# Optimization experiments

Hardware: AMD Instinct MI355X
Metric: run time of the kernel (lower is better)

The kernel has to match this reference:

```python
import jax, jax.numpy as jnp
import numpy as np

B, V, NQ, D, HEADS, FF, NL = 2, 8, 336, 256, 8, 1024, 6
H_IMG, W_IMG = 512, 512


def setup_inputs() -> dict:
    key = jax.random.key(0)
    ks = iter(jax.random.split(key, 48))
    def n(shape, s=0.02):
        return jax.random.normal(next(ks), shape, dtype=jnp.float32) * s
    inp = {}
    inp["tgt"] = jnp.zeros((B, NQ, D), jnp.float32)
    inp["query_pos"] = jax.random.normal(next(ks), (B, NQ, D), jnp.float32)
    inp["reference_points"] = jax.random.uniform(next(ks), (B, NQ, 3), dtype=jnp.float32)
    inp["feat0"] = jax.random.normal(next(ks), (B, V, D, 64, 64), jnp.float32)
    inp["feat1"] = jax.random.normal(next(ks), (B, V, D, 32, 32), jnp.float32)
    inp["feat2"] = jax.random.normal(next(ks), (B, V, D, 16, 16), jnp.float32)
    # cameras: near-identity rotations, translation pushed +2 in z so points project in front
    inp["camera_R"] = jnp.broadcast_to(jnp.eye(3, dtype=jnp.float32), (B, V, 3, 3)) + n((B, V, 3, 3), 0.1)
    T = n((B, V, 3), 0.1)
    inp["camera_T"] = T.at[..., 2].add(2.0)
    K = jnp.array([[500.0, 0.0, 256.0], [0.0, 500.0, 256.0], [0.0, 0.0, 1.0]], jnp.float32)
    inp["camera_K"] = jnp.broadcast_to(K, (B, V, 3, 3))
    # decoder params (stacked over NL layers)
    inp["Wqkv"] = n((NL, 3 * D, D)); inp["bqkv"] = jnp.zeros((NL, 3 * D), jnp.float32)
    inp["Wo"] = n((NL, D, D));       inp["bo"] = jnp.zeros((NL, D), jnp.float32)
    inp["ln1_g"] = jnp.ones((NL, D), jnp.float32); inp["ln1_b"] = jnp.zeros((NL, D), jnp.float32)
    inp["Wproj"] = n((NL, D, D));    inp["bproj"] = jnp.zeros((NL, D), jnp.float32)
    inp["pn_g"] = jnp.ones((NL, D), jnp.float32); inp["pn_b"] = jnp.zeros((NL, D), jnp.float32)
    inp["W1"] = n((NL, FF, D));      inp["b1"] = jnp.zeros((NL, FF), jnp.float32)
    inp["W2"] = n((NL, D, FF));      inp["b2"] = jnp.zeros((NL, D), jnp.float32)
    inp["ln2_g"] = jnp.ones((NL, D), jnp.float32); inp["ln2_b"] = jnp.zeros((NL, D), jnp.float32)
    inp["pose_W0"] = n((D, D)); inp["pose_b0"] = jnp.zeros((D,), jnp.float32)
    inp["pose_W1"] = n((D, D)); inp["pose_b1"] = jnp.zeros((D,), jnp.float32)
    inp["pose_W2"] = n((3, D)); inp["pose_b2"] = jnp.zeros((3,), jnp.float32)
    inp["cls_W"] = n((1, D));   inp["cls_b"] = jnp.zeros((1,), jnp.float32)
    return inp


def _layer_norm(x, g, b):
    m = x.mean(-1, keepdims=True)
    v = ((x - m) ** 2).mean(-1, keepdims=True)
    return (x - m) * jax.lax.rsqrt(v + 1e-5) * g + b


def _project(pts, R, T, K):
    # pts (B,NQ,3) -> cam coords per view: pts @ R^T + T
    p = jnp.einsum('bqc,bvdc->bvqd', pts, R) + T[:, :, None, :]  # (B,V,NQ,3)
    z = jnp.clip(p[..., 2], 0.1, None)
    fx = K[..., 0, 0][:, :, None]; fy = K[..., 1, 1][:, :, None]
    cx = K[..., 0, 2][:, :, None]; cy = K[..., 1, 2][:, :, None]
    u = p[..., 0] * fx / z + cx
    v = p[..., 1] * fy / z + cy
    un = 2.0 * u / (W_IMG - 1) - 1.0
    vn = 2.0 * v / (H_IMG - 1) - 1.0
    mask = (un > -1.0) & (un < 1.0) & (vn > -1.0) & (vn < 1.0) & (p[..., 2] > 0)
    return jnp.stack([un, vn], -1), mask  # (B,V,NQ,2), (B,V,NQ)


def _sample(feats, grid):
    # bilinear point sampling == F.grid_sample(align_corners=False, padding_mode='zeros')
    C, Hh, Ww = feats.shape[2], feats.shape[3], feats.shape[4]
    f = feats.reshape(B * V, C, Hh, Ww)
    g = grid.reshape(B * V, NQ, 2)
    x = (g[..., 0] + 1.0) * Ww * 0.5 - 0.5
    y = (g[..., 1] + 1.0) * Hh * 0.5 - 0.5
    x0f = jnp.floor(x); y0f = jnp.floor(y)
    ix0 = x0f.astype(jnp.int32); iy0 = y0f.astype(jnp.int32)
    ix1 = ix0 + 1; iy1 = iy0 + 1
    wx1 = (x - x0f)[:, None, :]; wx0 = 1.0 - wx1
    wy1 = (y - y0f)[:, None, :]; wy0 = 1.0 - wy1
    def gat(ix, iy):
        valid = ((ix >= 0) & (ix < Ww) & (iy >= 0) & (iy < Hh)).astype(f.dtype)[:, None, :]
        ixc = jnp.clip(ix, 0, Ww - 1); iyc = jnp.clip(iy, 0, Hh - 1)
        vals = jax.vmap(lambda ff, yy, xx: ff[:, yy, xx])(f, iyc, ixc)  # (BV,C,NQ)
        return vals * valid
    out = (gat(ix0, iy0) * wy0 * wx0 + gat(ix1, iy0) * wy0 * wx1 +
           gat(ix0, iy1) * wy1 * wx0 + gat(ix1, iy1) * wy1 * wx1)
    return out.reshape(B, V, C, NQ).transpose(0, 1, 3, 2)  # (B,V,NQ,C)


def _mha(xq, xv, Wqkv, bqkv, Wo, bo):
    hd = D // HEADS
    q = (xq @ Wqkv[:D].T + bqkv[:D]).reshape(B, NQ, HEADS, hd)
    k = (xq @ Wqkv[D:2 * D].T + bqkv[D:2 * D]).reshape(B, NQ, HEADS, hd)
    v = (xv @ Wqkv[2 * D:].T + bqkv[2 * D:]).reshape(B, NQ, HEADS, hd)
    att = jax.nn.softmax(jnp.einsum('bqhd,bkhd->bhqk', q, k) * (1.0 / np.sqrt(hd)), axis=-1)
    o = jnp.einsum('bhqk,bkhd->bqhd', att, v).reshape(B, NQ, D)
    return o @ Wo.T + bo


def reference(tgt, query_pos, reference_points, feat0, feat1, feat2, camera_R, camera_T, camera_K,
              Wqkv, bqkv, Wo, bo, ln1_g, ln1_b, Wproj, bproj, pn_g, pn_b,
              W1, b1, W2, b2, ln2_g, ln2_b,
              pose_W0, pose_b0, pose_W1, pose_b1, pose_W2, pose_b2, cls_W, cls_b):
    out = tgt
    ref = reference_points
    feats = (feat0, feat1, feat2)
    logits_all, poses_all = [], []
    for l in range(NL):
        # self-attention (dropout = eval identity)
        qk = out + query_pos
        out = _layer_norm(out + _mha(qk, out, Wqkv[l], bqkv[l], Wo[l], bo[l]), ln1_g[l], ln1_b[l])
        # projective attention: project 3D refs, grid-sample all levels, mask-fuse across views
        grid, mask = _project(ref, camera_R, camera_T, camera_K)
        ms = (_sample(feats[0], grid) + _sample(feats[1], grid) + _sample(feats[2], grid)) / 3.0
        vm = mask[..., None].astype(out.dtype)  # (B,V,NQ,1)
        fused = (ms * vm).sum(1) / jnp.clip(vm.sum(1), 1.0, None)  # (B,NQ,D)
        out = _layer_norm(out + fused @ Wproj[l].T + bproj[l], pn_g[l], pn_b[l])
        # FFN
        ffn = jax.nn.relu(out @ W1[l].T + b1[l]) @ W2[l].T + b2[l]
        out = _layer_norm(out + ffn, ln2_g[l], ln2_b[l])
        # iterative pose refinement + classification head
        h = jax.nn.relu(out @ pose_W0.T + pose_b0)
        h = jax.nn.relu(h @ pose_W1.T + pose_b1)
        ref = ref + h @ pose_W2.T + pose_b2
        logits_all.append(out @ cls_W.T + cls_b)
        poses_all.append(ref)
    # (NL,B,NQ,1) logits ++ (NL,B,NQ,3) poses -> (NL,B,NQ,4)
    return jnp.concatenate([jnp.stack(logits_all), jnp.stack(poses_all)], axis=-1)
```

## Files before the change

### kernel.cpp

```cpp
#include <hip/hip_runtime.h>
#include <math.h>

#define BB 2
#define VV 8
#define NQ 336
#define DD 256
#define HEADS 8
#define HD 32
#define FF 1024
#define NL 6
#define BQ (BB*NQ)
#define W_IMG 512
#define H_IMG 512
#define MROWS BQ

__device__ __forceinline__ void job_transpose3(float* tile, int b,
                                               const float* __restrict__ f0,
                                               const float* __restrict__ f1,
                                               const float* __restrict__ f2,
                                               float* __restrict__ o0,
                                               float* __restrict__ o1,
                                               float* __restrict__ o2) {
    const float* src; float* dst; int HW, ptiles;
    if (b < 4096)      { src = f0; dst = o0; HW = 4096; ptiles = 128; }
    else if (b < 5120) { b -= 4096; src = f1; dst = o1; HW = 1024; ptiles = 32; }
    else               { b -= 5120; src = f2; dst = o2; HW = 256;  ptiles = 8;  }
    int cg = b & 1;
    int pt = (b >> 1) % ptiles;
    int bv = (b >> 1) / ptiles;
    int d0 = cg * 128, p0 = pt * 32;
    int t = threadIdx.x;
    int chb = t >> 3, px4 = (t & 7) * 4;
    #pragma unroll
    for (int pass = 0; pass < 4; ++pass) {
        int ch = pass * 32 + chb;
        float4 v = *(const float4*)(src + ((size_t)(bv * DD + d0 + ch)) * HW + p0 + px4);
        tile[ch * 33 + px4 + 0] = v.x; tile[ch * 33 + px4 + 1] = v.y;
        tile[ch * 33 + px4 + 2] = v.z; tile[ch * 33 + px4 + 3] = v.w;
    }
    __syncthreads();
    int c4 = (t & 31) * 4, pxb = t >> 5;
    #pragma unroll
    for (int pass = 0; pass < 4; ++pass) {
        int px = pass * 8 + pxb;
        float4 o;
        o.x = tile[(c4 + 0) * 33 + px];
        o.y = tile[(c4 + 1) * 33 + px];
        o.z = tile[(c4 + 2) * 33 + px];
        o.w = tile[(c4 + 3) * 33 + px];
        *(float4*)(dst + ((size_t)bv * HW + p0 + px) * DD + d0 + c4) = o;
    }
}

__global__ __launch_bounds__(256) void init_k(const float* __restrict__ tgt,
                                              const float* __restrict__ qp,
                                              const float* __restrict__ refpts,
                                              float* __restrict__ x,
                                              float* __restrict__ xq,
                                              float* __restrict__ refb) {
    int i = blockIdx.x * 256 + threadIdx.x;
    float4 tv = ((const float4*)tgt)[i];
    float4 qv = ((const float4*)qp)[i];
    ((float4*)x)[i] = tv;
    ((float4*)xq)[i] = make_float4(tv.x + qv.x, tv.y + qv.y, tv.z + qv.z, tv.w + qv.w);
    if (i < BQ * 3) refb[i] = refpts[i];
}

__device__ __forceinline__ void job_qkv(float* sm, int bid,
                                        const float* __restrict__ Aq,
                                        const float* __restrict__ Ax,
                                        const float* __restrict__ W,
                                        const float* __restrict__ bias,
                                        float* __restrict__ Qp,
                                        float* __restrict__ Kp,
                                        float* __restrict__ Vp) {
    float* At = sm;
    float* Wt = sm + 1088;
    int t = threadIdx.x;
    int m0 = (bid % 21) * 32;
    int ncol = bid / 21;
    int n0 = ncol * 64;
    const float* A = (ncol < 8) ? Aq : Ax;
    int tx = t & 15, ty = t >> 4;
    int nc = n0 + tx * 4;
    float acc0[4], acc1[4];
    {
        float4 bv = *(const float4*)(bias + nc);
        acc0[0] = bv.x; acc0[1] = bv.y; acc0[2] = bv.z; acc0[3] = bv.w;
        acc1[0] = bv.x; acc1[1] = bv.y; acc1[2] = bv.z; acc1[3] = bv.w;
    }
    int am = t >> 3, ak4 = (t & 7) * 4;
    for (int kt = 0; kt < 8; ++kt) {
        int kk = kt * 32;
        __syncthreads();
        {
            float4 v = *(const float4*)(A + (size_t)(m0 + am) * DD + kk + ak4);
            At[(ak4 + 0) * 34 + am] = v.x; At[(ak4 + 1) * 34 + am] = v.y;
            At[(ak4 + 2) * 34 + am] = v.z; At[(ak4 + 3) * 34 + am] = v.w;
        }
        #pragma unroll
        for (int s = 0; s < 2; ++s) {
            int idx = t + s * 256;
            int wn = idx >> 3, wk4 = (idx & 7) * 4;
            float4 v = *(const float4*)(W + (size_t)(n0 + wn) * DD + kk + wk4);
            Wt[(wk4 + 0) * 68 + wn] = v.x; Wt[(wk4 + 1) * 68 + wn] = v.y;
            Wt[(wk4 + 2) * 68 + wn] = v.z; Wt[(wk4 + 3) * 68 + wn] = v.w;
        }
        __syncthreads();
        #pragma unroll
        for (int k = 0; k < 32; ++k) {
            float2 av = *(const float2*)&At[k * 34 + ty * 2];
            float4 wv = *(const float4*)&Wt[k * 68 + tx * 4];
            acc0[0] = fmaf(av.x, wv.x, acc0[0]); acc0[1] = fmaf(av.x, wv.y, acc0[1]);
            acc0[2] = fmaf(av.x, wv.z, acc0[2]); acc0[3] = fmaf(av.x, wv.w, acc0[3]);
            acc1[0] = fmaf(av.y, wv.x, acc1[0]); acc1[1] = fmaf(av.y, wv.y, acc1[1]);
            acc1[2] = fmaf(av.y, wv.z, acc1[2]); acc1[3] = fmaf(av.y, wv.w, acc1[3]);
        }
    }
    int mr = m0 + ty * 2;
    int kind = nc >> 8;
    float* base = kind == 0 ? Qp : (kind == 1 ? Kp : Vp);
    int h = (nc >> 5) & 7, d4 = nc & 31;
    #pragma unroll
    for (int i = 0; i < 2; ++i) {
        int m = mr + i;
        int b = m / NQ, q = m - b * NQ;
        float* p = base + ((size_t)((b << 3) + h) * NQ + q) * HD + d4;
        float* src = i == 0 ? acc0 : acc1;
        *(float4*)p = make_float4(src[0], src[1], src[2], src[3]);
    }
}

__device__ __forceinline__ void job_pose(float* sm, int job,
                                         const float* __restrict__ x,
                                         const float* __restrict__ W0, const float* __restrict__ b0,
                                         const float* __restrict__ W1p, const float* __restrict__ b1p,
                                         const float* __restrict__ W2p, const float* __restrict__ b2p,
                                         const float* __restrict__ cW, const float* __restrict__ cb,
                                         float* __restrict__ refb, float* __restrict__ outp) {
    float* sX  = sm;
    float* sH  = sm + 1024;
    float* red = sm + 2048;
    int r0 = job * 4;
    int tid = threadIdx.x;
    ((float4*)sX)[tid] = ((const float4*)(x + (size_t)r0 * DD))[tid];
    __syncthreads();
    {
        float a0 = b0[tid], a1 = a0, a2 = a0, a3 = a0;
        const float* wp = W0 + (size_t)tid * DD;
        for (int k = 0; k < DD; k += 4) {
            float4 w  = *(const float4*)(wp + k);
            float4 x0 = *(const float4*)(sX + 0 * DD + k);
            float4 x1 = *(const float4*)(sX + 1 * DD + k);
            float4 x2 = *(const float4*)(sX + 2 * DD + k);
            float4 x3 = *(const float4*)(sX + 3 * DD + k);
            a0 = fmaf(x0.x, w.x, a0); a0 = fmaf(x0.y, w.y, a0); a0 = fmaf(x0.z, w.z, a0); a0 = fmaf(x0.w, w.w, a0);
            a1 = fmaf(x1.x, w.x, a1); a1 = fmaf(x1.y, w.y, a1); a1 = fmaf(x1.z, w.z, a1); a1 = fmaf(x1.w, w.w, a1);
            a2 = fmaf(x2.x, w.x, a2); a2 = fmaf(x2.y, w.y, a2); a2 = fmaf(x2.z, w.z, a2); a2 = fmaf(x2.w, w.w, a2);
            a3 = fmaf(x3.x, w.x, a3); a3 = fmaf(x3.y, w.y, a3); a3 = fmaf(x3.z, w.z, a3); a3 = fmaf(x3.w, w.w, a3);
        }
        sH[0 * DD + tid] = fmaxf(a0, 0.f);
        sH[1 * DD + tid] = fmaxf(a1, 0.f);
        sH[2 * DD + tid] = fmaxf(a2, 0.f);
        sH[3 * DD + tid] = fmaxf(a3, 0.f);
    }
    __syncthreads();
    float h[4];
    {
        float a0 = b1p[tid], a1 = a0, a2 = a0, a3 = a0;
        const float* wp = W1p + (size_t)tid * DD;
        for (int k = 0; k < DD; k += 4) {
            float4 w  = *(const float4*)(wp + k);
            float4 x0 = *(const float4*)(sH + 0 * DD + k);
            float4 x1 = *(const float4*)(sH + 1 * DD + k);
            float4 x2 = *(const float4*)(sH + 2 * DD + k);
            float4 x3 = *(const float4*)(sH + 3 * DD + k);
            a0 = fmaf(x0.x, w.x, a0); a0 = fmaf(x0.y, w.y, a0); a0 = fmaf(x0.z, w.z, a0); a0 = fmaf(x0.w, w.w, a0);
            a1 = fmaf(x1.x, w.x, a1); a1 = fmaf(x1.y, w.y, a1); a1 = fmaf(x1.z, w.z, a1); a1 = fmaf(x1.w, w.w, a1);
            a2 = fmaf(x2.x, w.x, a2); a2 = fmaf(x2.y, w.y, a2); a2 = fmaf(x2.z, w.z, a2); a2 = fmaf(x2.w, w.w, a2);
            a3 = fmaf(x3.x, w.x, a3); a3 = fmaf(x3.y, w.y, a3); a3 = fmaf(x3.z, w.z, a3); a3 = fmaf(x3.w, w.w, a3);
        }
        h[0] = fmaxf(a0, 0.f); h[1] = fmaxf(a1, 0.f); h[2] = fmaxf(a2, 0.f); h[3] = fmaxf(a3, 0.f);
    }
    float w2a = W2p[tid], w2b = W2p[DD + tid], w2c = W2p[2 * DD + tid], cw = cW[tid];
    float v[4][4];
    #pragma unroll
    for (int r = 0; r < 4; ++r) {
        v[r][0] = h[r] * w2a;
        v[r][1] = h[r] * w2b;
        v[r][2] = h[r] * w2c;
        v[r][3] = sX[r * DD + tid] * cw;
    }
    #pragma unroll
    for (int o2 = 32; o2 > 0; o2 >>= 1) {
        #pragma unroll
        for (int r = 0; r < 4; ++r) {
            #pragma unroll
            for (int c = 0; c < 4; ++c) v[r][c] += __shfl_xor(v[r][c], o2);
        }
    }
    int wid = tid >> 6, lane = tid & 63;
    if (lane == 0) {
        #pragma unroll
        for (int r = 0; r < 4; ++r) {
            #pragma unroll
            for (int c = 0; c < 4; ++c) red[(r * 4 + c) * 4 + wid] = v[r][c];
        }
    }
    __syncthreads();
    if (tid < 4) {
        int r = tid;
        float d0 = red[(r * 4 + 0) * 4 + 0] + red[(r * 4 + 0) * 4 + 1] + red[(r * 4 + 0) * 4 + 2] + red[(r * 4 + 0) * 4 + 3] + b2p[0];
        float d1 = red[(r * 4 + 1) * 4 + 0] + red[(r * 4 + 1) * 4 + 1] + red[(r * 4 + 1) * 4 + 2] + red[(r * 4 + 1) * 4 + 3] + b2p[1];
        float d2 = red[(r * 4 + 2) * 4 + 0] + red[(r * 4 + 2) * 4 + 1] + red[(r * 4 + 2) * 4 + 2] + red[(r * 4 + 2) * 4 + 3] + b2p[2];
        float cl = red[(r * 4 + 3) * 4 + 0] + red[(r * 4 + 3) * 4 + 1] + red[(r * 4 + 3) * 4 + 2] + red[(r * 4 + 3) * 4 + 3] + cb[0];
        int row = r0 + r;
        float rx = refb[(size_t)row * 3 + 0] + d0;
        float ry = refb[(size_t)row * 3 + 1] + d1;
        float rz = refb[(size_t)row * 3 + 2] + d2;
        refb[(size_t)row * 3 + 0] = rx;
        refb[(size_t)row * 3 + 1] = ry;
        refb[(size_t)row * 3 + 2] = rz;
        outp[(size_t)row * 4 + 0] = cl;
        outp[(size_t)row * 4 + 1] = rx;
        outp[(size_t)row * 4 + 2] = ry;
        outp[(size_t)row * 4 + 3] = rz;
    }
}

__global__ __launch_bounds__(256) void qkv_pose(const float* __restrict__ xq,
                                                const float* __restrict__ x,
                                                const float* __restrict__ Wqkv,
                                                const float* __restrict__ bqkv,
                                                float* __restrict__ Qp,
                                                float* __restrict__ Kp,
                                                float* __restrict__ Vp,
                                                const float* __restrict__ pW0, const float* __restrict__ pb0,
                                                const float* __restrict__ pW1, const float* __restrict__ pb1,
                                                const float* __restrict__ pW2, const float* __restrict__ pb2,
                                                const float* __restrict__ cW, const float* __restrict__ cb,
                                                float* __restrict__ refb, float* __restrict__ outp) {
    __shared__ float sm[3264];
    if (blockIdx.x < 252)
        job_qkv(sm, blockIdx.x, xq, x, Wqkv, bqkv, Qp, Kp, Vp);
    else
        job_pose(sm, blockIdx.x - 252, x, pW0, pb0, pW1, pb1, pW2, pb2, cW, cb, refb, outp);
}

__global__ __launch_bounds__(256) void qkv_tr(const float* __restrict__ xq,
                                              const float* __restrict__ x,
                                              const float* __restrict__ Wqkv,
                                              const float* __restrict__ bqkv,
                                              float* __restrict__ Qp,
                                              float* __restrict__ Kp,
                                              float* __restrict__ Vp,
                                              const float* __restrict__ f0,
                                              const float* __restrict__ f1,
                                              const float* __restrict__ f2,
                                              float* __restrict__ o0,
                                              float* __restrict__ o1,
                                              float* __restrict__ o2) {
    __shared__ float sm[4224];
    if (blockIdx.x < 252)
        job_qkv(sm, blockIdx.x, xq, x, Wqkv, bqkv, Qp, Kp, Vp);
    else
        job_transpose3(sm, blockIdx.x - 252, f0, f1, f2, o0, o1, o2);
}

__global__ __launch_bounds__(256) void pose_only(const float* __restrict__ x,
                                                 const float* __restrict__ pW0, const float* __restrict__ pb0,
                                                 const float* __restrict__ pW1, const float* __restrict__ pb1,
                                                 const float* __restrict__ pW2, const float* __restrict__ pb2,
                                                 const float* __restrict__ cW, const float* __restrict__ cb,
                                                 float* __restrict__ refb, float* __restrict__ outp) {
    __shared__ float sm[2112];
    job_pose(sm, blockIdx.x, x, pW0, pb0, pW1, pb1, pW2, pb2, cW, cb, refb, outp);
}

__global__ __launch_bounds__(256) void attn16(const float* __restrict__ Qp,
                                              const float* __restrict__ Kp,
                                              const float* __restrict__ Vp,
                                              float* __restrict__ O) {
    __shared__ float sm[9744];
    float* S   = sm;
    float* KT  = sm + 5504;
    float* U   = sm + 7680;
    float* inv = sm + 9728;
    int blk = blockIdx.x;
    int bh = blk & 15, qt = blk >> 4;
    int t = threadIdx.x;
    const float scale = 0.17677669529663687f;
    const float* Qb = Qp + (size_t)bh * NQ * HD;
    const float* Kb = Kp + (size_t)bh * NQ * HD;
    const float* Vb = Vp + (size_t)bh * NQ * HD;
    if (t < 128) {
        int ql = t >> 3, d4 = (t & 7) * 4;
        int qg = qt * 16 + ql;
        float4 v = (qg < NQ) ? *(const float4*)(Qb + (size_t)qg * HD + d4)
                             : make_float4(0.f, 0.f, 0.f, 0.f);
        U[(d4 + 0) * 20 + ql] = v.x * scale;
        U[(d4 + 1) * 20 + ql] = v.y * scale;
        U[(d4 + 2) * 20 + ql] = v.z * scale;
        U[(d4 + 3) * 20 + ql] = v.w * scale;
    }
    int r = t >> 4, tx = t & 15;
    for (int kt = 0; kt < 6; ++kt) {
        __syncthreads();
        #pragma unroll
        for (int s = 0; s < 2; ++s) {
            int idx = t + s * 256;
            int kl = idx >> 3, d4 = (idx & 7) * 4;
            int kg = kt * 64 + kl;
            float4 v = (kg < NQ) ? *(const float4*)(Kb + (size_t)kg * HD + d4)
                                 : make_float4(0.f, 0.f, 0.f, 0.f);
            KT[(d4 + 0) * 68 + kl] = v.x; KT[(d4 + 1) * 68 + kl] = v.y;
            KT[(d4 + 2) * 68 + kl] = v.z; KT[(d4 + 3) * 68 + kl] = v.w;
        }
        __syncthreads();
        float a0 = 0.f, a1 = 0.f, a2 = 0.f, a3 = 0.f;
        #pragma unroll
        for (int k = 0; k < 32; ++k) {
            float qv = U[k * 20 + r];
            float4 kv = *(const float4*)&KT[k * 68 + tx * 4];
            a0 = fmaf(qv, kv.x, a0); a1 = fmaf(qv, kv.y, a1);
            a2 = fmaf(qv, kv.z, a2); a3 = fmaf(qv, kv.w, a3);
        }
        int col = kt * 64 + tx * 4;
        if (col < NQ)
            *(float4*)&S[r * 344 + col] = make_float4(a0, a1, a2, a3);
    }
    __syncthreads();
    {
        float* row = S + (size_t)r * 344;
        float m = -1e30f;
        for (int i = 0; i < 21; ++i) m = fmaxf(m, row[tx + 16 * i]);
        m = fmaxf(m, __shfl_xor(m, 1));
        m = fmaxf(m, __shfl_xor(m, 2));
        m = fmaxf(m, __shfl_xor(m, 4));
        m = fmaxf(m, __shfl_xor(m, 8));
        float ssum = 0.f;
        for (int i = 0; i < 21; ++i) {
            float e = expf(row[tx + 16 * i] - m);
            row[tx + 16 * i] = e;
            ssum += e;
        }
        ssum += __shfl_xor(ssum, 1);
        ssum += __shfl_xor(ssum, 2);
        ssum += __shfl_xor(ssum, 4);
        ssum += __shfl_xor(ssum, 8);
        if (tx == 0) inv[r] = 1.f / ssum;
    }
    int d0 = tx * 2;
    float acc0 = 0.f, acc1 = 0.f;
    for (int kt = 0; kt < 6; ++kt) {
        __syncthreads();
        #pragma unroll
        for (int s = 0; s < 2; ++s) {
            int idx = t + s * 256;
            int kl = idx >> 3, d4 = (idx & 7) * 4;
            int kg = kt * 64 + kl;
            float4 v = (kg < NQ) ? *(const float4*)(Vb + (size_t)kg * HD + d4)
                                 : make_float4(0.f, 0.f, 0.f, 0.f);
            *(float4*)&U[kl * 32 + d4] = v;
        }
        __syncthreads();
        int kmax = (kt == 5) ? 16 : 64;
        const float* Srow = S + (size_t)r * 344 + kt * 64;
        #pragma unroll 8
        for (int kk = 0; kk < kmax; ++kk) {
            float p = Srow[kk];
            float2 vv = *(const float2*)&U[kk * 32 + d0];
            acc0 = fmaf(p, vv.x, acc0); acc1 = fmaf(p, vv.y, acc1);
        }
    }
    float iv = inv[r];
    int qg = qt * 16 + r;
    int b = bh >> 3, h = bh & 7;
    if (qg < NQ)
        *(float2*)(O + ((size_t)(b * NQ + qg)) * DD + h * HD + d0) =
            make_float2(acc0 * iv, acc1 * iv);
}

__device__ __forceinline__ void job_gemm_ln(float* sm, int r0,
                                            const float* __restrict__ A,
                                            const float* __restrict__ Wt,
                                            const float* __restrict__ bias,
                                            const float* __restrict__ gam,
                                            const float* __restrict__ bet,
                                            float* __restrict__ x) {
    float* sA    = sm;
    float* redS  = sm + 1024;
    float* redS2 = sm + 1040;
    float* mu    = sm + 1056;
    float* ri    = sm + 1060;
    int j = threadIdx.x;
    ((float4*)sA)[j] = ((const float4*)(A + (size_t)r0 * DD))[j];
    __syncthreads();
    float acc0 = bias[j], acc1 = acc0, acc2 = acc0, acc3 = acc0;
    const float* wp = Wt + (size_t)j * DD;
    for (int k = 0; k < DD; k += 4) {
        float4 w  = *(const float4*)(wp + k);
        float4 a0 = *(const float4*)(sA + 0 * DD + k);
        float4 a1 = *(const float4*)(sA + 1 * DD + k);
        float4 a2 = *(const float4*)(sA + 2 * DD + k);
        float4 a3 = *(const float4*)(sA + 3 * DD + k);
        acc0 = fmaf(a0.x, w.x, acc0); acc0 = fmaf(a0.y, w.y, acc0); acc0 = fmaf(a0.z, w.z, acc0); acc0 = fmaf(a0.w, w.w, acc0);
        acc1 = fmaf(a1.x, w.x, acc1); acc1 = fmaf(a1.y, w.y, acc1); acc1 = fmaf(a1.z, w.z, acc1); acc1 = fmaf(a1.w, w.w, acc1);
        acc2 = fmaf(a2.x, w.x, acc2); acc2 = fmaf(a2.y, w.y, acc2); acc2 = fmaf(a2.z, w.z, acc2); acc2 = fmaf(a2.w, w.w, acc2);
        acc3 = fmaf(a3.x, w.x, acc3); acc3 = fmaf(a3.y, w.y, acc3); acc3 = fmaf(a3.z, w.z, acc3); acc3 = fmaf(a3.w, w.w, acc3);
    }
    float val[4];
    val[0] = x[(size_t)(r0 + 0) * DD + j] + acc0;
    val[1] = x[(size_t)(r0 + 1) * DD + j] + acc1;
    val[2] = x[(size_t)(r0 + 2) * DD + j] + acc2;
    val[3] = x[(size_t)(r0 + 3) * DD + j] + acc3;
    float s[4], s2[4];
    #pragma unroll
    for (int r = 0; r < 4; ++r) { s[r] = val[r]; s2[r] = val[r] * val[r]; }
    #pragma unroll
    for (int o2 = 32; o2 > 0; o2 >>= 1) {
        #pragma unroll
        for (int r = 0; r < 4; ++r) {
            s[r]  += __shfl_xor(s[r],  o2);
            s2[r] += __shfl_xor(s2[r], o2);
        }
    }
    int wid = j >> 6, lane = j & 63;
    if (lane == 0) {
        #pragma unroll
        for (int r = 0; r < 4; ++r) { redS[r * 4 + wid] = s[r]; redS2[r * 4 + wid] = s2[r]; }
    }
    __syncthreads();
    if (j < 4) {
// ... 68 lines not shown
                int ix = ix0 + (tap & 1);
                int iy = iy0 + (tap >> 1);
                float wgt = ((tap & 1) ? wx1 : wx0) * ((tap >> 1) ? wy1 : wy0);
                if (ix >= 0 && ix < Ww && iy >= 0 && iy < Hh) {
                    if (TRANSPOSED) {
                        const float* p = f + ((size_t)bv * Hh * Ww + (size_t)iy * Ww + ix) * DD + ch0;
                        float4 va = *(const float4*)p;
                        float4 vb = *(const float4*)(p + 4);
                        acc[0] = fmaf(wgt, va.x, acc[0]); acc[1] = fmaf(wgt, va.y, acc[1]);
                        acc[2] = fmaf(wgt, va.z, acc[2]); acc[3] = fmaf(wgt, va.w, acc[3]);
                        acc[4] = fmaf(wgt, vb.x, acc[4]); acc[5] = fmaf(wgt, vb.y, acc[5]);
                        acc[6] = fmaf(wgt, vb.z, acc[6]); acc[7] = fmaf(wgt, vb.w, acc[7]);
                    } else {
                        #pragma unroll
                        for (int c = 0; c < 8; ++c) {
                            float vv2 = f[(((size_t)bv * DD + ch0 + c) * Hh + iy) * Ww + ix];
                            acc[c] = fmaf(wgt, vv2, acc[c]);
                        }
                    }
                }
            }
        }
    }
    #pragma unroll
    for (int c = 0; c < 8; ++c) sPart[v * 258 + ch0 + c] = acc[c] * (1.f / 3.f);
    __syncthreads();
    float cnt = sg[2] + sg[5] + sg[8] + sg[11] + sg[14] + sg[17] + sg[20] + sg[23];
    float s = 0.f;
    #pragma unroll
    for (int v2 = 0; v2 < 8; ++v2) s += sPart[v2 * 258 + t];
    fused[(size_t)row * DD + t] = s / fmaxf(cnt, 1.f);
}

template <bool TRANSPOSED>
__global__ __launch_bounds__(256) void oproj_sample(const float* __restrict__ attn_o,
                                                    const float* __restrict__ Wo,
                                                    const float* __restrict__ bo,
                                                    const float* __restrict__ gam,
                                                    const float* __restrict__ bet,
                                                    float* __restrict__ x,
                                                    const float* __restrict__ f0,
                                                    const float* __restrict__ f1,
                                                    const float* __restrict__ f2,
                                                    const float* __restrict__ refb,
                                                    const float* __restrict__ Rm,
                                                    const float* __restrict__ Tm,
                                                    const float* __restrict__ Km,
                                                    float* __restrict__ fused) {
    __shared__ float sm[2112];
    if (blockIdx.x < 168)
        job_gemm_ln(sm, blockIdx.x * 4, attn_o, Wo, bo, gam, bet, x);
    else
        job_sample<TRANSPOSED>(sm, blockIdx.x - 168, f0, f1, f2, refb, Rm, Tm, Km, fused);
}

template <int MODE>
__global__ __launch_bounds__(256) void gemm_tile(const float* __restrict__ A,
                                                 const float* __restrict__ W,
                                                 const float* __restrict__ bias,
                                                 float* __restrict__ C,
                                                 int Ktot, int Kper, int Nout) {
    __shared__ float At[32][34];
    __shared__ float Wt[32][68];
    int t = threadIdx.x;
    int m0 = blockIdx.x * 32;
    int n0 = blockIdx.y * 64;
    int kz = blockIdx.z;
    int kofs = kz * Kper;
    int tx = t & 15, ty = t >> 4;
    int nc = n0 + tx * 4;
    float acc0[4], acc1[4];
    {
        float4 bv = make_float4(0.f, 0.f, 0.f, 0.f);
        if (bias && kz == 0) bv = *(const float4*)(bias + nc);
        acc0[0] = bv.x; acc0[1] = bv.y; acc0[2] = bv.z; acc0[3] = bv.w;
        acc1[0] = bv.x; acc1[1] = bv.y; acc1[2] = bv.z; acc1[3] = bv.w;
    }
    int am = t >> 3, ak4 = (t & 7) * 4;
    int ktiles = Kper >> 5;
    for (int kt = 0; kt < ktiles; ++kt) {
        int kk = kofs + kt * 32;
        __syncthreads();
        {
            float4 v = *(const float4*)(A + (size_t)(m0 + am) * Ktot + kk + ak4);
            At[ak4 + 0][am] = v.x; At[ak4 + 1][am] = v.y;
            At[ak4 + 2][am] = v.z; At[ak4 + 3][am] = v.w;
        }
        #pragma unroll
        for (int s = 0; s < 2; ++s) {
            int idx = t + s * 256;
            int wn = idx >> 3, wk4 = (idx & 7) * 4;
            float4 v = *(const float4*)(W + (size_t)(n0 + wn) * Ktot + kk + wk4);
            Wt[wk4 + 0][wn] = v.x; Wt[wk4 + 1][wn] = v.y;
            Wt[wk4 + 2][wn] = v.z; Wt[wk4 + 3][wn] = v.w;
        }
        __syncthreads();
        #pragma unroll
        for (int k = 0; k < 32; ++k) {
            float2 av = *(const float2*)&At[k][ty * 2];
            float4 wv = *(const float4*)&Wt[k][tx * 4];
            acc0[0] = fmaf(av.x, wv.x, acc0[0]); acc0[1] = fmaf(av.x, wv.y, acc0[1]);
            acc0[2] = fmaf(av.x, wv.z, acc0[2]); acc0[3] = fmaf(av.x, wv.w, acc0[3]);
            acc1[0] = fmaf(av.y, wv.x, acc1[0]); acc1[1] = fmaf(av.y, wv.y, acc1[1]);
            acc1[2] = fmaf(av.y, wv.z, acc1[2]); acc1[3] = fmaf(av.y, wv.w, acc1[3]);
        }
    }
    if (MODE == 1) {
        #pragma unroll
        for (int j = 0; j < 4; ++j) { acc0[j] = fmaxf(acc0[j], 0.f); acc1[j] = fmaxf(acc1[j], 0.f); }
    }
    int mr = m0 + ty * 2;
    float* Cb = C + (size_t)kz * MROWS * Nout;
    *(float4*)(Cb + (size_t)mr * Nout + nc)       = make_float4(acc0[0], acc0[1], acc0[2], acc0[3]);
    *(float4*)(Cb + (size_t)(mr + 1) * Nout + nc) = make_float4(acc1[0], acc1[1], acc1[2], acc1[3]);
}

template <int NP>
__global__ __launch_bounds__(256) void ln_res(float* __restrict__ x,
                                              const float* __restrict__ C,
                                              const float* __restrict__ gam,
                                              const float* __restrict__ bet,
                                              const float* __restrict__ qp,
                                              float* __restrict__ xq) {
    __shared__ float redS[4][4], redS2[4][4];
    __shared__ float mu[4], ri[4];
    int r0 = blockIdx.x * 4;
    int j = threadIdx.x;
    float val[4];
    #pragma unroll
    for (int r = 0; r < 4; ++r) {
        float a = x[(size_t)(r0 + r) * DD + j];
        #pragma unroll
        for (int p = 0; p < NP; ++p) a += C[(size_t)p * MROWS * DD + (size_t)(r0 + r) * DD + j];
        val[r] = a;
    }
    float s[4], s2[4];
    #pragma unroll
    for (int r = 0; r < 4; ++r) { s[r] = val[r]; s2[r] = val[r] * val[r]; }
    #pragma unroll
    for (int o = 32; o > 0; o >>= 1) {
        #pragma unroll
        for (int r = 0; r < 4; ++r) {
            s[r]  += __shfl_xor(s[r],  o);
            s2[r] += __shfl_xor(s2[r], o);
        }
    }
    int wid = j >> 6, lane = j & 63;
    if (lane == 0) {
        #pragma unroll
        for (int r = 0; r < 4; ++r) { redS[r][wid] = s[r]; redS2[r][wid] = s2[r]; }
    }
    __syncthreads();
    if (j < 4) {
        int r = j;
        float ts  = redS[r][0]  + redS[r][1]  + redS[r][2]  + redS[r][3];
        float ts2 = redS2[r][0] + redS2[r][1] + redS2[r][2] + redS2[r][3];
        float mean = ts * (1.f / DD);
        float var = ts2 * (1.f / DD) - mean * mean;
        mu[r] = mean;
        ri[r] = rsqrtf(var + 1e-5f);
    }
    __syncthreads();
    float g = gam[j], be = bet[j];
    #pragma unroll
    for (int r = 0; r < 4; ++r) {
        float o = (val[r] - mu[r]) * ri[r] * g + be;
        x[(size_t)(r0 + r) * DD + j] = o;
// ... 2 lines not shown
}

extern "C" void kernel_launch(void* const* d_in, const int* in_sizes, int n_in,
                              void* d_out, int out_size, void* d_ws, size_t ws_size,
                              hipStream_t stream) {
    const float* tgt       = (const float*)d_in[0];
    const float* query_pos = (const float*)d_in[1];
    const float* refpts    = (const float*)d_in[2];
    const float* feat0     = (const float*)d_in[3];
    const float* feat1     = (const float*)d_in[4];
    const float* feat2     = (const float*)d_in[5];
    const float* camR      = (const float*)d_in[6];
    const float* camT      = (const float*)d_in[7];
    const float* camK      = (const float*)d_in[8];
    const float* Wqkv      = (const float*)d_in[9];
    const float* bqkv      = (const float*)d_in[10];
    const float* Wo        = (const float*)d_in[11];
    const float* bo        = (const float*)d_in[12];
    const float* ln1_g     = (const float*)d_in[13];
    const float* ln1_b     = (const float*)d_in[14];
    const float* Wproj     = (const float*)d_in[15];
    const float* bproj     = (const float*)d_in[16];
    const float* pn_g      = (const float*)d_in[17];
    const float* pn_b      = (const float*)d_in[18];
    const float* W1        = (const float*)d_in[19];
    const float* b1        = (const float*)d_in[20];
    const float* W2        = (const float*)d_in[21];
    const float* b2        = (const float*)d_in[22];
    const float* ln2_g     = (const float*)d_in[23];
    const float* ln2_b     = (const float*)d_in[24];
    const float* pose_W0   = (const float*)d_in[25];
    const float* pose_b0   = (const float*)d_in[26];
    const float* pose_W1   = (const float*)d_in[27];
    const float* pose_b1   = (const float*)d_in[28];
    const float* pose_W2   = (const float*)d_in[29];
    const float* pose_b2   = (const float*)d_in[30];
    const float* cls_W     = (const float*)d_in[31];
    const float* cls_b     = (const float*)d_in[32];
    float* out = (float*)d_out;

    float* w = (float*)d_ws;
    size_t off = 0;
    auto alloc = [&](size_t n) { float* p = w + off; off += n; return p; };
    float* x      = alloc((size_t)BQ * DD);
    float* xq     = alloc((size_t)BQ * DD);
    float* Qp     = alloc((size_t)BB * HEADS * NQ * HD);
    float* Kp     = alloc((size_t)BB * HEADS * NQ * HD);
    float* Vp     = alloc((size_t)BB * HEADS * NQ * HD);
    float* attn_o = alloc((size_t)BQ * DD);
    float* fused  = alloc((size_t)BQ * DD);
    float* ffh    = alloc((size_t)BQ * FF);
    float* ctmp   = alloc((size_t)4 * BQ * DD);
    float* refb   = alloc((size_t)BQ * 3 + 64);
    size_t base_floats = off;
    size_t featT_floats = (size_t)BB * VV * DD * (64 * 64 + 32 * 32 + 16 * 16);
    bool useT = ws_size >= (base_floats + featT_floats) * sizeof(float);
    float *fT0 = nullptr, *fT1 = nullptr, *fT2 = nullptr;
    if (useT) {
        fT0 = alloc((size_t)BB * VV * 64 * 64 * DD);
        fT1 = alloc((size_t)BB * VV * 32 * 32 * DD);
        fT2 = alloc((size_t)BB * VV * 16 * 16 * DD);
    }

    init_k<<<168, 256, 0, stream>>>(tgt, query_pos, refpts, x, xq, refb);

    for (int l = 0; l < NL; ++l) {
        if (l == 0 && useT) {
            qkv_tr<<<252 + 5376, 256, 0, stream>>>(
                xq, x, Wqkv, bqkv, Qp, Kp, Vp,
                feat0, feat1, feat2, fT0, fT1, fT2);
        } else {
            qkv_pose<<<252 + (l > 0 ? 168 : 0), 256, 0, stream>>>(
                xq, x, Wqkv + (size_t)l * 3 * DD * DD, bqkv + (size_t)l * 3 * DD, Qp, Kp, Vp,
                pose_W0, pose_b0, pose_W1, pose_b1, pose_W2, pose_b2, cls_W, cls_b,
                refb, out + (size_t)(l - 1) * BQ * 4);
        }
        attn16<<<352, 256, 0, stream>>>(Qp, Kp, Vp, attn_o);
        if (useT)
            oproj_sample<true><<<840, 256, 0, stream>>>(
                attn_o, Wo + (size_t)l * DD * DD, bo + (size_t)l * DD,
                ln1_g + (size_t)l * DD, ln1_b + (size_t)l * DD, x,
                fT0, fT1, fT2, refb, camR, camT, camK, fused);
        else
            oproj_sample<false><<<840, 256, 0, stream>>>(
                attn_o, Wo + (size_t)l * DD * DD, bo + (size_t)l * DD,
                ln1_g + (size_t)l * DD, ln1_b + (size_t)l * DD, x,
                feat0, feat1, feat2, refb, camR, camT, camK, fused);
        gemm_tile<0><<<dim3(21, 4, 4), 256, 0, stream>>>(
            fused, Wproj + (size_t)l * DD * DD, bproj + (size_t)l * DD, ctmp, DD, DD / 4, DD);
        ln_res<4><<<BQ / 4, 256, 0, stream>>>(
            x, ctmp, pn_g + (size_t)l * DD, pn_b + (size_t)l * DD, nullptr, nullptr);
        gemm_tile<1><<<dim3(21, 16, 1), 256, 0, stream>>>(
            x, W1 + (size_t)l * FF * DD, b1 + (size_t)l * FF, ffh, DD, DD, FF);
        gemm_tile<0><<<dim3(21, 4, 4), 256, 0, stream>>>(
            ffh, W2 + (size_t)l * DD * FF, b2 + (size_t)l * DD, ctmp, FF, FF / 4, DD);
        ln_res<4><<<BQ / 4, 256, 0, stream>>>(
            x, ctmp, ln2_g + (size_t)l * DD, ln2_b + (size_t)l * DD, query_pos, xq);
    }
    pose_only<<<BQ / 4, 256, 0, stream>>>(
        x, pose_W0, pose_b0, pose_W1, pose_b1, pose_W2, pose_b2, cls_W, cls_b,
        refb, out + (size_t)(NL - 1) * BQ * 4);
}
```

Before: 806.4 us.

## Split pose MLP into tiled GEMM jobs fused into qkv and attention kernels

Replaces the per-row pose-refinement block, which re-read both full pose weight matrices for every 4 rows, with tiled GEMM jobs. The first pose layer rides in the qkv kernel and the second in the attention kernel, followed by a small pose_heads kernel for the final projection and classifier. This is meant to cut redundant weight traffic and spread the pose work across existing launches. It adds one extra kernel launch per layer and at the end, and reuses the ctmp scratch buffer for intermediates.

```diff
diff --git a/kernel.cpp b/kernel.cpp
--- a/kernel.cpp
+++ b/kernel.cpp
@@ -64,6 +64,77 @@
     ((float4*)x)[i] = tv;
     ((float4*)xq)[i] = make_float4(tv.x + qv.x, tv.y + qv.y, tv.z + qv.z, tv.w + qv.w);
     if (i < BQ * 3) refb[i] = refpts[i];
+}
+
+template <int MODE>
+__device__ __forceinline__ void job_gemm_tile(float* sm, int bx, int by, int bz,
+                                              const float* __restrict__ A,
+                                              const float* __restrict__ W,
+                                              const float* __restrict__ bias,
+                                              float* __restrict__ C,
+                                              int Ktot, int Kper, int Nout) {
+    float* At = sm;
+    float* Wt = sm + 1088;
+    int t = threadIdx.x;
+    int m0 = bx * 32;
+    int n0 = by * 64;
+    int kofs = bz * Kper;
+    int tx = t & 15, ty = t >> 4;
+    int nc = n0 + tx * 4;
+    float acc0[4], acc1[4];
+    {
+        float4 bv = make_float4(0.f, 0.f, 0.f, 0.f);
+        if (bias && bz == 0) bv = *(const float4*)(bias + nc);
+        acc0[0] = bv.x; acc0[1] = bv.y; acc0[2] = bv.z; acc0[3] = bv.w;
+        acc1[0] = bv.x; acc1[1] = bv.y; acc1[2] = bv.z; acc1[3] = bv.w;
+    }
+    int am = t >> 3, ak4 = (t & 7) * 4;
+    int ktiles = Kper >> 5;
+    for (int kt = 0; kt < ktiles; ++kt) {
+        int kk = kofs + kt * 32;
+        __syncthreads();
+        {
+            float4 v = *(const float4*)(A + (size_t)(m0 + am) * Ktot + kk + ak4);
+            At[(ak4 + 0) * 34 + am] = v.x; At[(ak4 + 1) * 34 + am] = v.y;
+            At[(ak4 + 2) * 34 + am] = v.z; At[(ak4 + 3) * 34 + am] = v.w;
+        }
+        #pragma unroll
+        for (int s = 0; s < 2; ++s) {
+            int idx = t + s * 256;
+            int wn = idx >> 3, wk4 = (idx & 7) * 4;
+            float4 v = *(const float4*)(W + (size_t)(n0 + wn) * Ktot + kk + wk4);
+            Wt[(wk4 + 0) * 68 + wn] = v.x; Wt[(wk4 + 1) * 68 + wn] = v.y;
+            Wt[(wk4 + 2) * 68 + wn] = v.z; Wt[(wk4 + 3) * 68 + wn] = v.w;
+        }
+        __syncthreads();
+        #pragma unroll
+        for (int k = 0; k < 32; ++k) {
+            float2 av = *(const float2*)&At[k * 34 + ty * 2];
+            float4 wv = *(const float4*)&Wt[k * 68 + tx * 4];
+            acc0[0] = fmaf(av.x, wv.x, acc0[0]); acc0[1] = fmaf(av.x, wv.y, acc0[1]);
+            acc0[2] = fmaf(av.x, wv.z, acc0[2]); acc0[3] = fmaf(av.x, wv.w, acc0[3]);
+            acc1[0] = fmaf(av.y, wv.x, acc1[0]); acc1[1] = fmaf(av.y, wv.y, acc1[1]);
+            acc1[2] = fmaf(av.y, wv.z, acc1[2]); acc1[3] = fmaf(av.y, wv.w, acc1[3]);
+        }
+    }
+    if (MODE == 1) {
+        #pragma unroll
+        for (int j = 0; j < 4; ++j) { acc0[j] = fmaxf(acc0[j], 0.f); acc1[j] = fmaxf(acc1[j], 0.f); }
+    }
+    int mr = m0 + ty * 2;
+    float* Cb = C + (size_t)bz * MROWS * Nout;
+    *(float4*)(Cb + (size_t)mr * Nout + nc)       = make_float4(acc0[0], acc0[1], acc0[2], acc0[3]);
+    *(float4*)(Cb + (size_t)(mr + 1) * Nout + nc) = make_float4(acc1[0], acc1[1], acc1[2], acc1[3]);
+}
+
+template <int MODE>
+__global__ __launch_bounds__(256) void gemm_tile(const float* __restrict__ A,
+                                                 const float* __restrict__ W,
+                                                 const float* __restrict__ bias,
+                                                 float* __restrict__ C,
+                                                 int Ktot, int Kper, int Nout) {
+    __shared__ float sm[3264];
+    job_gemm_tile<MODE>(sm, blockIdx.x, blockIdx.y, blockIdx.z, A, W, bias, C, Ktot, Kper, Nout);
 }
 
 __device__ __forceinline__ void job_qkv(float* sm, int bid,
@@ -131,120 +202,23 @@
     }
 }
 
-__device__ __forceinline__ void job_pose(float* sm, int job,
-                                         const float* __restrict__ x,
-                                         const float* __restrict__ W0, const float* __restrict__ b0,
-                                         const float* __restrict__ W1p, const float* __restrict__ b1p,
-                                         const float* __restrict__ W2p, const float* __restrict__ b2p,
-                                         const float* __restrict__ cW, const float* __restrict__ cb,
-                                         float* __restrict__ refb, float* __restrict__ outp) {
-    float* sX  = sm;
-    float* sH  = sm + 1024;
-    float* red = sm + 2048;
-    int r0 = job * 4;
-    int tid = threadIdx.x;
-    ((float4*)sX)[tid] = ((const float4*)(x + (size_t)r0 * DD))[tid];
-    __syncthreads();
-    {
-        float a0 = b0[tid], a1 = a0, a2 = a0, a3 = a0;
-        const float* wp = W0 + (size_t)tid * DD;
-        for (int k = 0; k < DD; k += 4) {
-            float4 w  = *(const float4*)(wp + k);
-            float4 x0 = *(const float4*)(sX + 0 * DD + k);
-            float4 x1 = *(const float4*)(sX + 1 * DD + k);
-            float4 x2 = *(const float4*)(sX + 2 * DD + k);
-            float4 x3 = *(const float4*)(sX + 3 * DD + k);
-            a0 = fmaf(x0.x, w.x, a0); a0 = fmaf(x0.y, w.y, a0); a0 = fmaf(x0.z, w.z, a0); a0 = fmaf(x0.w, w.w, a0);
-            a1 = fmaf(x1.x, w.x, a1); a1 = fmaf(x1.y, w.y, a1); a1 = fmaf(x1.z, w.z, a1); a1 = fmaf(x1.w, w.w, a1);
-            a2 = fmaf(x2.x, w.x, a2); a2 = fmaf(x2.y, w.y, a2); a2 = fmaf(x2.z, w.z, a2); a2 = fmaf(x2.w, w.w, a2);
-            a3 = fmaf(x3.x, w.x, a3); a3 = fmaf(x3.y, w.y, a3); a3 = fmaf(x3.z, w.z, a3); a3 = fmaf(x3.w, w.w, a3);
-        }
-        sH[0 * DD + tid] = fmaxf(a0, 0.f);
-        sH[1 * DD + tid] = fmaxf(a1, 0.f);
-        sH[2 * DD + tid] = fmaxf(a2, 0.f);
-        sH[3 * DD + tid] = fmaxf(a3, 0.f);
-    }
-    __syncthreads();
-    float h[4];
-    {
-        float a0 = b1p[tid], a1 = a0, a2 = a0, a3 = a0;
-        const float* wp = W1p + (size_t)tid * DD;
-        for (int k = 0; k < DD; k += 4) {
-            float4 w  = *(const float4*)(wp + k);
-            float4 x0 = *(const float4*)(sH + 0 * DD + k);
-            float4 x1 = *(const float4*)(sH + 1 * DD + k);
-            float4 x2 = *(const float4*)(sH + 2 * DD + k);
-            float4 x3 = *(const float4*)(sH + 3 * DD + k);
-            a0 = fmaf(x0.x, w.x, a0); a0 = fmaf(x0.y, w.y, a0); a0 = fmaf(x0.z, w.z, a0); a0 = fmaf(x0.w, w.w, a0);
-            a1 = fmaf(x1.x, w.x, a1); a1 = fmaf(x1.y, w.y, a1); a1 = fmaf(x1.z, w.z, a1); a1 = fmaf(x1.w, w.w, a1);
-            a2 = fmaf(x2.x, w.x, a2); a2 = fmaf(x2.y, w.y, a2); a2 = fmaf(x2.z, w.z, a2); a2 = fmaf(x2.w, w.w, a2);
-            a3 = fmaf(x3.x, w.x, a3); a3 = fmaf(x3.y, w.y, a3); a3 = fmaf(x3.z, w.z, a3); a3 = fmaf(x3.w, w.w, a3);
-        }
-        h[0] = fmaxf(a0, 0.f); h[1] = fmaxf(a1, 0.f); h[2] = fmaxf(a2, 0.f); h[3] = fmaxf(a3, 0.f);
-    }
-    float w2a = W2p[tid], w2b = W2p[DD + tid], w2c = W2p[2 * DD + tid], cw = cW[tid];
-    float v[4][4];
-    #pragma unroll
-    for (int r = 0; r < 4; ++r) {
-        v[r][0] = h[r] * w2a;
-        v[r][1] = h[r] * w2b;
-        v[r][2] = h[r] * w2c;
-        v[r][3] = sX[r * DD + tid] * cw;
-    }
-    #pragma unroll
-    for (int o2 = 32; o2 > 0; o2 >>= 1) {
-        #pragma unroll
-        for (int r = 0; r < 4; ++r) {
-            #pragma unroll
-            for (int c = 0; c < 4; ++c) v[r][c] += __shfl_xor(v[r][c], o2);
-        }
-    }
-    int wid = tid >> 6, lane = tid & 63;
-    if (lane == 0) {
-        #pragma unroll
-        for (int r = 0; r < 4; ++r) {
-            #pragma unroll
-            for (int c = 0; c < 4; ++c) red[(r * 4 + c) * 4 + wid] = v[r][c];
-        }
-    }
-    __syncthreads();
-    if (tid < 4) {
-        int r = tid;
-        float d0 = red[(r * 4 + 0) * 4 + 0] + red[(r * 4 + 0) * 4 + 1] + red[(r * 4 + 0) * 4 + 2] + red[(r * 4 + 0) * 4 + 3] + b2p[0];
-        float d1 = red[(r * 4 + 1) * 4 + 0] + red[(r * 4 + 1) * 4 + 1] + red[(r * 4 + 1) * 4 + 2] + red[(r * 4 + 1) * 4 + 3] + b2p[1];
-        float d2 = red[(r * 4 + 2) * 4 + 0] + red[(r * 4 + 2) * 4 + 1] + red[(r * 4 + 2) * 4 + 2] + red[(r * 4 + 2) * 4 + 3] + b2p[2];
-        float cl = red[(r * 4 + 3) * 4 + 0] + red[(r * 4 + 3) * 4 + 1] + red[(r * 4 + 3) * 4 + 2] + red[(r * 4 + 3) * 4 + 3] + cb[0];
-        int row = r0 + r;
-        float rx = refb[(size_t)row * 3 + 0] + d0;
-        float ry = refb[(size_t)row * 3 + 1] + d1;
-        float rz = refb[(size_t)row * 3 + 2] + d2;
-        refb[(size_t)row * 3 + 0] = rx;
-        refb[(size_t)row * 3 + 1] = ry;
-        refb[(size_t)row * 3 + 2] = rz;
-        outp[(size_t)row * 4 + 0] = cl;
-        outp[(size_t)row * 4 + 1] = rx;
-        outp[(size_t)row * 4 + 2] = ry;
-        outp[(size_t)row * 4 + 3] = rz;
-    }
-}
-
-__global__ __launch_bounds__(256) void qkv_pose(const float* __restrict__ xq,
-                                                const float* __restrict__ x,
-                                                const float* __restrict__ Wqkv,
-                                                const float* __restrict__ bqkv,
-                                                float* __restrict__ Qp,
-                                                float* __restrict__ Kp,
-                                                float* __restrict__ Vp,
-                                                const float* __restrict__ pW0, const float* __restrict__ pb0,
-                                                const float* __restrict__ pW1, const float* __restrict__ pb1,
-                                                const float* __restrict__ pW2, const float* __restrict__ pb2,
-                                                const float* __restrict__ cW, const float* __restrict__ cb,
-                                                float* __restrict__ refb, float* __restrict__ outp) {
+__global__ __launch_bounds__(256) void qkv_g1(const float* __restrict__ xq,
+                                              const float* __restrict__ x,
+                                              const float* __restrict__ Wqkv,
+                                              const float* __restrict__ bqkv,
+                                              float* __restrict__ Qp,
+                                              float* __restrict__ Kp,
+                                              float* __restrict__ Vp,
+                                              const float* __restrict__ pW0,
+                                              const float* __restrict__ pb0,
+                                              float* __restrict__ ph1) {
     __shared__ float sm[3264];
     if (blockIdx.x < 252)
         job_qkv(sm, blockIdx.x, xq, x, Wqkv, bqkv, Qp, Kp, Vp);
-    else
-        job_pose(sm, blockIdx.x - 252, x, pW0, pb0, pW1, pb1, pW2, pb2, cW, cb, refb, outp);
+    else {
+        int id = blockIdx.x - 252;
+        job_gemm_tile<1>(sm, id % 21, id / 21, 0, x, pW0, pb0, ph1, DD, DD, DD);
+    }
 }
 
 __global__ __launch_bounds__(256) void qkv_tr(const float* __restrict__ xq,
@@ -267,26 +241,15 @@
         job_transpose3(sm, blockIdx.x - 252, f0, f1, f2, o0, o1, o2);
 }
 
-__global__ __launch_bounds__(256) void pose_only(const float* __restrict__ x,
-                                                 const float* __restrict__ pW0, const float* __restrict__ pb0,
-                                                 const float* __restrict__ pW1, const float* __restrict__ pb1,
-                                                 const float* __restrict__ pW2, const float* __restrict__ pb2,
-                                                 const float* __restrict__ cW, const float* __restrict__ cb,
-                                                 float* __restrict__ refb, float* __restrict__ outp) {
-    __shared__ float sm[2112];
-    job_pose(sm, blockIdx.x, x, pW0, pb0, pW1, pb1, pW2, pb2, cW, cb, refb, outp);
-}
-
-__global__ __launch_bounds__(256) void attn16(const float* __restrict__ Qp,
-                                              const float* __restrict__ Kp,
-                                              const float* __restrict__ Vp,
-                                              float* __restrict__ O) {
-    __shared__ float sm[9744];
+__device__ __forceinline__ void job_attn16(float* sm, int blk,
+                                           const float* __restrict__ Qp,
+                                           const float* __restrict__ Kp,
+                                           const float* __restrict__ Vp,
+                                           float* __restrict__ O) {
     float* S   = sm;
     float* KT  = sm + 5504;
     float* U   = sm + 7680;
     float* inv = sm + 9728;
-    int blk = blockIdx.x;
     int bh = blk & 15, qt = blk >> 4;
     int t = threadIdx.x;
     const float scale = 0.17677669529663687f;
@@ -379,6 +342,86 @@
     if (qg < NQ)
         *(float2*)(O + ((size_t)(b * NQ + qg)) * DD + h * HD + d0) =
             make_float2(acc0 * iv, acc1 * iv);
+}
+
+__global__ __launch_bounds__(256) void attn16_g2(const float* __restrict__ Qp,
+                                                 const float* __restrict__ Kp,
+                                                 const float* __restrict__ Vp,
+                                                 float* __restrict__ O,
+                                                 const float* __restrict__ ph1,
+                                                 const float* __restrict__ pW1,
+                                                 const float* __restrict__ pb1,
+                                                 float* __restrict__ ph2) {
+    __shared__ float sm[9744];
+    if (blockIdx.x < 352)
+        job_attn16(sm, blockIdx.x, Qp, Kp, Vp, O);
+    else {
+        int id = blockIdx.x - 352;
+        job_gemm_tile<1>(sm, id % 21, id / 21, 0, ph1, pW1, pb1, ph2, DD, DD, DD);
+    }
+}
+
+__global__ __launch_bounds__(256) void pose_heads(const float* __restrict__ x,
+                                                  const float* __restrict__ ph2,
+                                                  const float* __restrict__ W2p,
+                                                  const float* __restrict__ b2p,
+                                                  const float* __restrict__ cW,
+                                                  const float* __restrict__ cb,
+                                                  float* __restrict__ refb,
+                                                  float* __restrict__ outp) {
+    __shared__ float sX[1024];
+    __shared__ float red[64];
+    int r0 = blockIdx.x * 4;
+    int tid = threadIdx.x;
+    ((float4*)sX)[tid] = ((const float4*)(x + (size_t)r0 * DD))[tid];
+    float h[4];
+    #pragma unroll
+    for (int r = 0; r < 4; ++r) h[r] = ph2[(size_t)(r0 + r) * DD + tid];
+    __syncthreads();
+    float w2a = W2p[tid], w2b = W2p[DD + tid], w2c = W2p[2 * DD + tid], cw = cW[tid];
+    float v[4][4];
+    #pragma unroll
+    for (int r = 0; r < 4; ++r) {
+        v[r][0] = h[r] * w2a;
+        v[r][1] = h[r] * w2b;
+        v[r][2] = h[r] * w2c;
+        v[r][3] = sX[r * DD + tid] * cw;
+    }
+    #pragma unroll
+    for (int o2 = 32; o2 > 0; o2 >>= 1) {
+        #pragma unroll
+        for (int r = 0; r < 4; ++r) {
+            #pragma unroll
+            for (int c = 0; c < 4; ++c) v[r][c] += __shfl_xor(v[r][c], o2);
+        }
+    }
+    int wid = tid >> 6, lane = tid & 63;
+    if (lane == 0) {
+        #pragma unroll
+        for (int r = 0; r < 4; ++r) {
+            #pragma unroll
+            for (int c = 0; c < 4; ++c) red[(r * 4 + c) * 4 + wid] = v[r][c];
+        }
+    }
+    __syncthreads();
+    if (tid < 4) {
+        int r = tid;
+        float d0 = red[(r * 4 + 0) * 4 + 0] + red[(r * 4 + 0) * 4 + 1] + red[(r * 4 + 0) * 4 + 2] + red[(r * 4 + 0) * 4 + 3] + b2p[0];
+        float d1 = red[(r * 4 + 1) * 4 + 0] + red[(r * 4 + 1) * 4 + 1] + red[(r * 4 + 1) * 4 + 2] + red[(r * 4 + 1) * 4 + 3] + b2p[1];
+        float d2 = red[(r * 4 + 2) * 4 + 0] + red[(r * 4 + 2) * 4 + 1] + red[(r * 4 + 2) * 4 + 2] + red[(r * 4 + 2) * 4 + 3] + b2p[2];
+        float cl = red[(r * 4 + 3) * 4 + 0] + red[(r * 4 + 3) * 4 + 1] + red[(r * 4 + 3) * 4 + 2] + red[(r * 4 + 3) * 4 + 3] + cb[0];
+        int row = r0 + r;
+        float rx = refb[(size_t)row * 3 + 0] + d0;
+        float ry = refb[(size_t)row * 3 + 1] + d1;
+        float rz = refb[(size_t)row * 3 + 2] + d2;
+        refb[(size_t)row * 3 + 0] = rx;
+        refb[(size_t)row * 3 + 1] = ry;
+        refb[(size_t)row * 3 + 2] = rz;
+        outp[(size_t)row * 4 + 0] = cl;
+        outp[(size_t)row * 4 + 1] = rx;
+        outp[(size_t)row * 4 + 2] = ry;
+        outp[(size_t)row * 4 + 3] = rz;
+    }
 }
 
 __device__ __forceinline__ void job_gemm_ln(float* sm, int r0,
@@ -553,67 +596,6 @@
         job_gemm_ln(sm, blockIdx.x * 4, attn_o, Wo, bo, gam, bet, x);
     else
         job_sample<TRANSPOSED>(sm, blockIdx.x - 168, f0, f1, f2, refb, Rm, Tm, Km, fused);
-}
-
-template <int MODE>
-__global__ __launch_bounds__(256) void gemm_tile(const float* __restrict__ A,
-                                                 const float* __restrict__ W,
-                                                 const float* __restrict__ bias,
-                                                 float* __restrict__ C,
-                                                 int Ktot, int Kper, int Nout) {
-    __shared__ float At[32][34];
-    __shared__ float Wt[32][68];
-    int t = threadIdx.x;
-    int m0 = blockIdx.x * 32;
-    int n0 = blockIdx.y * 64;
-    int kz = blockIdx.z;
-    int kofs = kz * Kper;
-    int tx = t & 15, ty = t >> 4;
-    int nc = n0 + tx * 4;
-    float acc0[4], acc1[4];
-    {
-        float4 bv = make_float4(0.f, 0.f, 0.f, 0.f);
-        if (bias && kz == 0) bv = *(const float4*)(bias + nc);
-        acc0[0] = bv.x; acc0[1] = bv.y; acc0[2] = bv.z; acc0[3] = bv.w;
-        acc1[0] = bv.x; acc1[1] = bv.y; acc1[2] = bv.z; acc1[3] = bv.w;
-    }
-    int am = t >> 3, ak4 = (t & 7) * 4;
-    int ktiles = Kper >> 5;
-    for (int kt = 0; kt < ktiles; ++kt) {
-        int kk = kofs + kt * 32;
-        __syncthreads();
-        {
-            float4 v = *(const float4*)(A + (size_t)(m0 + am) * Ktot + kk + ak4);
-            At[ak4 + 0][am] = v.x; At[ak4 + 1][am] = v.y;
-            At[ak4 + 2][am] = v.z; At[ak4 + 3][am] = v.w;
-        }
-        #pragma unroll
-        for (int s = 0; s < 2; ++s) {
-            int idx = t + s * 256;
-            int wn = idx >> 3, wk4 = (idx & 7) * 4;
-            float4 v = *(const float4*)(W + (size_t)(n0 + wn) * Ktot + kk + wk4);
-            Wt[wk4 + 0][wn] = v.x; Wt[wk4 + 1][wn] = v.y;
-            Wt[wk4 + 2][wn] = v.z; Wt[wk4 + 3][wn] = v.w;
-        }
-        __syncthreads();
-        #pragma unroll
-        for (int k = 0; k < 32; ++k) {
-            float2 av = *(const float2*)&At[k][ty * 2];
-            float4 wv = *(const float4*)&Wt[k][tx * 4];
-            acc0[0] = fmaf(av.x, wv.x, acc0[0]); acc0[1] = fmaf(av.x, wv.y, acc0[1]);
-            acc0[2] = fmaf(av.x, wv.z, acc0[2]); acc0[3] = fmaf(av.x, wv.w, acc0[3]);
-            acc1[0] = fmaf(av.y, wv.x, acc1[0]); acc1[1] = fmaf(av.y, wv.y, acc1[1]);
-            acc1[2] = fmaf(av.y, wv.z, acc1[2]); acc1[3] = fmaf(av.y, wv.w, acc1[3]);
-        }
-    }
-    if (MODE == 1) {
-        #pragma unroll
-        for (int j = 0; j < 4; ++j) { acc0[j] = fmaxf(acc0[j], 0.f); acc1[j] = fmaxf(acc1[j], 0.f); }
-    }
-    int mr = m0 + ty * 2;
-    float* Cb = C + (size_t)kz * MROWS * Nout;
-    *(float4*)(Cb + (size_t)mr * Nout + nc)       = make_float4(acc0[0], acc0[1], acc0[2], acc0[3]);
-    *(float4*)(Cb + (size_t)(mr + 1) * Nout + nc) = make_float4(acc1[0], acc1[1], acc1[2], acc1[3]);
 }
 
 template <int NP>
@@ -722,6 +704,8 @@
     float* ffh    = alloc((size_t)BQ * FF);
     float* ctmp   = alloc((size_t)4 * BQ * DD);
     float* refb   = alloc((size_t)BQ * 3 + 64);
+    float* ph1 = ctmp;
+    float* ph2 = ctmp + (size_t)BQ * DD;
     size_t base_floats = off;
     size_t featT_floats = (size_t)BB * VV * DD * (64 * 64 + 32 * 32 + 16 * 16);
     bool useT = ws_size >= (base_floats + featT_floats) * sizeof(float);
@@ -740,12 +724,15 @@
                 xq, x, Wqkv, bqkv, Qp, Kp, Vp,
                 feat0, feat1, feat2, fT0, fT1, fT2);
         } else {
-            qkv_pose<<<252 + (l > 0 ? 168 : 0), 256, 0, stream>>>(
+            qkv_g1<<<252 + (l > 0 ? 84 : 0), 256, 0, stream>>>(
                 xq, x, Wqkv + (size_t)l * 3 * DD * DD, bqkv + (size_t)l * 3 * DD, Qp, Kp, Vp,
-                pose_W0, pose_b0, pose_W1, pose_b1, pose_W2, pose_b2, cls_W, cls_b,
-                refb, out + (size_t)(l - 1) * BQ * 4);
-        }
-        attn16<<<352, 256, 0, stream>>>(Qp, Kp, Vp, attn_o);
+                pose_W0, pose_b0, ph1);
+        }
+        attn16_g2<<<352 + (l > 0 ? 84 : 0), 256, 0, stream>>>(
+            Qp, Kp, Vp, attn_o, ph1, pose_W1, pose_b1, ph2);
+        if (l > 0)
+            pose_heads<<<BQ / 4, 256, 0, stream>>>(
+                x, ph2, pose_W2, pose_b2, cls_W, cls_b, refb, out + (size_t)(l - 1) * BQ * 4);
         if (useT)
             oproj_sample<true><<<840, 256, 0, stream>>>(
                 attn_o, Wo + (size_t)l * DD * DD, bo + (size_t)l * DD,
@@ -767,7 +754,10 @@
         ln_res<4><<<BQ / 4, 256, 0, stream>>>(
             x, ctmp, ln2_g + (size_t)l * DD, ln2_b + (size_t)l * DD, query_pos, xq);
     }
-    pose_only<<<BQ / 4, 256, 0, stream>>>(
-        x, pose_W0, pose_b0, pose_W1, pose_b1, pose_W2, pose_b2, cls_W, cls_b,
-        refb, out + (size_t)(NL - 1) * BQ * 4);
-}
+    gemm_tile<1><<<dim3(21, 4, 1), 256, 0, stream>>>(
+        x, pose_W0, pose_b0, ph1, DD, DD, DD);
+    gemm_tile<1><<<dim3(21, 4, 1), 256, 0, stream>>>(
+        ph1, pose_W1, pose_b1, ph2, DD, DD, DD);
+    pose_heads<<<BQ / 4, 256, 0, stream>>>(
+        x, ph2, pose_W2, pose_b2, cls_W, cls_b, refb, out + (size_t)(NL - 1) * BQ * 4);
+}
```

Measured after the change: 809.7 us. Within noise of the previous version (+0.4%).
